# Performance work log

Measured on AMD Instinct MI355X. Metric: run time of the kernel, lower is better.

## Reference

```python
import jax, jax.numpy as jnp
import numpy as np

B, S, H, P, T = 8, 2048, 1024, 256, 4
EPS = 1e-12


def setup_inputs() -> dict:
    key = jax.random.key(0)
    ks = jax.random.split(key, 12)
    sd = 0.02
    return {
        "hidden_states": jax.random.normal(ks[0], (B, S, H), jnp.float32),
        "input_tensor": jax.random.normal(ks[1], (B, S, H), jnp.float32),
        "attention_mask": jnp.zeros((B, 1, 1, S), jnp.float32),
        "dense_W": jax.random.normal(ks[2], (H, H), jnp.float32) * sd,
        "dense_b": jnp.zeros((H,), jnp.float32),
        "pal_W1": jax.random.normal(ks[3], (T, H, P), jnp.float32) * sd,  # H2L per task
        "pal_b1": jnp.zeros((T, P), jnp.float32),
        "pal_W2": jax.random.normal(ks[4], (T, P, H), jnp.float32) * sd,  # L2H per task
        "pal_b2": jnp.zeros((T, H), jnp.float32),
        "enc_W": jax.random.normal(ks[5], (H,), jnp.float32) * sd,  # Linear(H,1)
        "enc_b": jnp.zeros((), jnp.float32),
        "sel_W": jax.random.normal(ks[6], (T, H), jnp.float32) * sd,  # Linear(H,T)
        "sel_b": jnp.zeros((T,), jnp.float32),
        "ln_g": jnp.ones((H,), jnp.float32),
        "ln_b": jnp.zeros((H,), jnp.float32),
    }


def reference(hidden_states, input_tensor, attention_mask, dense_W, dense_b,
              pal_W1, pal_b1, pal_W2, pal_b2, enc_W, enc_b, sel_W, sel_b,
              ln_g, ln_b):
    # dense projection (dropout p=0 -> identity)
    h = jnp.einsum('bsh,hk->bsk', hidden_states, dense_W) + dense_b  # [B,S,H]

    # per-task PAL adapters: H -> P -> H, stacked over T
    low = jnp.einsum('bsh,thp->btsp', h, pal_W1) + pal_b1[:, None, :]   # [B,T,S,P]
    task_specific = jnp.einsum('btsp,tph->btsh', low, pal_W2) + pal_b2[:, None, :]  # [B,T,S,H]

    # token-level gating: softmax over sequence of (encoder logits + additive mask)
    task_logits = jnp.einsum('bsh,h->bs', h, enc_W) + enc_b            # [B,S]
    task_weights = jax.nn.softmax(task_logits + attention_mask.reshape(B, S), axis=-1)
    task_vector = jnp.einsum('bs,bsh->bh', task_weights, h)            # [B,H]

    # task selector distribution and weighted combine over task branches
    task_distribution = jax.nn.softmax(task_vector @ sel_W.T + sel_b, axis=-1)  # [B,T]
    summed = jnp.einsum('btsh,bt->bsh', task_specific, task_distribution)       # [B,S,H]

    # residual + LayerNorm (eps=1e-12)
    x = h + input_tensor + summed
    mu = x.mean(-1, keepdims=True)
    var = ((x - mu) ** 2).mean(-1, keepdims=True)
    return ln_g * (x - mu) / jnp.sqrt(var + EPS) + ln_b
```

## Files before the change

kernel.cpp:

```cpp
#include <hip/hip_runtime.h>
#include <stdint.h>

#define DEVI __device__ __forceinline__

typedef __attribute__((ext_vector_type(8))) short s8v;
typedef __attribute__((ext_vector_type(4))) float f4v;
typedef unsigned short u16;

DEVI float bf2f(u16 u) { union { uint32_t i; float f; } c; c.i = ((uint32_t)u) << 16; return c.f; }
DEVI u16 f2bf(float f) {
  union { float f; uint32_t u; } c; c.f = f;
  uint32_t u = c.u;
  u += 0x7fffu + ((u >> 16) & 1u);
  return (u16)(u >> 16);
}

DEVI void gld16(const void* g, void* l) {
  auto gp = reinterpret_cast<const __attribute__((address_space(1))) void*>(reinterpret_cast<uintptr_t>(g));
  auto lp = reinterpret_cast<__attribute__((address_space(3))) void*>(reinterpret_cast<uintptr_t>(l));
  __builtin_amdgcn_global_load_lds(gp, lp, 16, 0, 0);
}

DEVI float wredsum(float v) {
  #pragma unroll
  for (int o = 32; o; o >>= 1) v += __shfl_xor(v, o);
  return v;
}

#define MFMA16(a, b, c) __builtin_amdgcn_mfma_f32_16x16x32_bf16((a), (b), (c), 0, 0, 0)

__global__ void cvt_f32_bf16(const float4* __restrict__ in, ushort4* __restrict__ out) {
  int i = blockIdx.x * 256 + threadIdx.x;
  float4 v = in[i];
  ushort4 o;
  o.x = f2bf(v.x); o.y = f2bf(v.y); o.z = f2bf(v.z); o.w = f2bf(v.w);
  out[i] = o;
}

__global__ void transpose_cvt(const float* __restrict__ in, u16* __restrict__ out, int R, int C) {
  __shared__ float t[32][33];
  in  += (size_t)blockIdx.z * R * C;
  out += (size_t)blockIdx.z * R * C;
  int r0 = blockIdx.y * 32, c0 = blockIdx.x * 32;
  int tx = threadIdx.x, ty = threadIdx.y;
  #pragma unroll
  for (int j = ty; j < 32; j += 8) t[j][tx] = in[(size_t)(r0 + j) * C + c0 + tx];
  __syncthreads();
  #pragma unroll
  for (int j = ty; j < 32; j += 8) out[(size_t)(c0 + j) * R + r0 + tx] = f2bf(t[tx][j]);
}


template<int EPI>
__global__ __launch_bounds__(256, 4) void gemm_bt(
    const u16* __restrict__ A, const u16* __restrict__ Bt, void* out,
    const float* __restrict__ e0, const float* __restrict__ e1, const u16* e2)
{
  const int tid  = threadIdx.x;
  const int lane = tid & 63;
  const int wv   = tid >> 6;
  const int wg = ((blockIdx.x & 7) << 7) | (blockIdx.x >> 3);
  const int tm = wg >> 3;
  const int tn = wg & 7;

  __shared__ char lds[32768];
  char* As = lds;
  char* Bs = lds + 16384;

  f4v acc[4][4];
  #pragma unroll
  for (int i = 0; i < 4; i++)
    #pragma unroll
    for (int j = 0; j < 4; j++) acc[i][j] = f4v{0.f, 0.f, 0.f, 0.f};

  const int wr = wv >> 1, wc = wv & 1;
  const int mB = wr * 64, nB = wc * 64;
  const int fr = lane & 15;
  const int fkbyte = (lane >> 4) << 4;

  const char* Ab = (const char*)(A + (size_t)tm * 128 * 1024);
  const char* Bb = (const char*)(Bt + (size_t)tn * 128 * 1024);

  for (int k0 = 0; k0 < 1024; k0 += 64) {
    #pragma unroll
    for (int c = 0; c < 4; ++c) {
      int p = wv * 1024 + lane * 16 + c * 4096;
      int row = p >> 7;
      int kb = (p & 127) ^ ((row & 7) << 4);
      gld16(Ab + (size_t)row * 2048 + k0 * 2 + kb, As + p);
      gld16(Bb + (size_t)row * 2048 + k0 * 2 + kb, Bs + p);
    }
    __syncthreads();
    #pragma unroll
    for (int kk = 0; kk < 2; ++kk) {
      s8v af[4], bf[4];
      #pragma unroll
      for (int i = 0; i < 4; ++i) {
        int ra = mB + i * 16 + fr;
        int rb = nB + i * 16 + fr;
        int kbyte = kk * 64 + fkbyte;
        af[i] = *(const s8v*)(As + ra * 128 + (kbyte ^ ((ra & 7) << 4)));
        bf[i] = *(const s8v*)(Bs + rb * 128 + (kbyte ^ ((rb & 7) << 4)));
      }
      #pragma unroll
      for (int mi = 0; mi < 4; ++mi)
        #pragma unroll
        for (int ni = 0; ni < 4; ++ni)
          acc[mi][ni] = MFMA16(af[mi], bf[ni], acc[mi][ni]);
    }
    __syncthreads();
  }

  const int mBase = tm * 128 + mB;
  const int nBase = tn * 128 + nB;
  const int rl = (lane >> 4) << 2;
  const int cl = lane & 15;
  float scale = 0.f;
  const float* b2row = nullptr;
  if constexpr (EPI == 2) scale = e1[(tm >> 4) * 4 + (tn >> 1)];
  if constexpr (EPI == 3) b2row = e0 + (tm >> 4) * 1024;

  #pragma unroll
  for (int mi = 0; mi < 4; ++mi) {
    #pragma unroll
    for (int ni = 0; ni < 4; ++ni) {
      int n = nBase + ni * 16 + cl;
      #pragma unroll
      for (int v = 0; v < 4; ++v) {
        int m = mBase + mi * 16 + rl + v;
        size_t idx = (size_t)m * 1024 + n;
        float val = acc[mi][ni][v];
        if constexpr (EPI == 1) {
          ((u16*)out)[idx] = f2bf(val + e0[n]);
        } else if constexpr (EPI == 2) {
          ((u16*)out)[idx] = f2bf(scale * (val + e0[n]));
        } else {
          ((u16*)out)[idx] = f2bf(val + b2row[n] + bf2f(e2[idx]) + e1[idx]);
        }
      }
    }
  }
}

template<int EPI>
__global__ __launch_bounds__(512, 6) void gemm_hi(
    const u16* __restrict__ A, const u16* __restrict__ Bt, void* out,
    const float* __restrict__ e0, const float* __restrict__ e1, const u16* e2)
{
  const int tid  = threadIdx.x;
  const int lane = tid & 63;
  const int wid  = tid >> 6;
  const int wm = wid >> 1, wn = wid & 1;
  const int wg = ((blockIdx.x & 7) << 7) | (blockIdx.x >> 3);
  const int tm = wg >> 3;
  const int tn = wg & 7;

  __shared__ char As[16384];
  __shared__ char Bs[16384];

  f4v acc[2][4];
  #pragma unroll
  for (int i = 0; i < 2; i++)
    #pragma unroll
    for (int j = 0; j < 4; j++) acc[i][j] = f4v{0.f, 0.f, 0.f, 0.f};

  const int mB = wm * 32, nB = wn * 64;
  const int fr = lane & 15;
  const int fkbyte = (lane >> 4) << 4;

  const char* Ab = (const char*)(A + (size_t)tm * 128 * 1024);
  const char* Bb = (const char*)(Bt + (size_t)tn * 128 * 1024);

  for (int k0 = 0; k0 < 1024; k0 += 64) {
    #pragma unroll
    for (int c = 0; c < 2; ++c) {
      int p = tid * 16 + c * 8192;
      int row = p >> 7;
      int kb = (p & 127) ^ ((row & 7) << 4);
      gld16(Ab + (size_t)row * 2048 + k0 * 2 + kb, As + p);
      gld16(Bb + (size_t)row * 2048 + k0 * 2 + kb, Bs + p);
    }
    __syncthreads();
    #pragma unroll
    for (int kk = 0; kk < 2; ++kk) {
      s8v af[2], bf[4];
      const int kbyte = kk * 64 + fkbyte;
      #pragma unroll
      for (int i = 0; i < 2; ++i) {
        int ra = mB + i * 16 + fr;
        af[i] = *(const s8v*)(As + ra * 128 + (kbyte ^ ((ra & 7) << 4)));
      }
      #pragma unroll
      for (int j = 0; j < 4; ++j) {
        int rb = nB + j * 16 + fr;
        bf[j] = *(const s8v*)(Bs + rb * 128 + (kbyte ^ ((rb & 7) << 4)));
      }
      #pragma unroll
      for (int i = 0; i < 2; ++i)
        #pragma unroll
        for (int j = 0; j < 4; ++j)
          acc[i][j] = MFMA16(af[i], bf[j], acc[i][j]);
    }
    __syncthreads();
  }

  const int mBase = tm * 128 + mB;
  const int nBase = tn * 128 + nB;
  const int rl = (lane >> 4) << 2;
  const int cl = lane & 15;
  float scale = 0.f;
  const float* b2row = nullptr;
  if constexpr (EPI == 2) scale = e1[(tm >> 4) * 4 + (tn >> 1)];
  if constexpr (EPI == 3) b2row = e0 + (tm >> 4) * 1024;

  #pragma unroll
  for (int i = 0; i < 2; ++i) {
    #pragma unroll
    for (int j = 0; j < 4; ++j) {
      int n = nBase + j * 16 + cl;
      #pragma unroll
      for (int v = 0; v < 4; ++v) {
        int m = mBase + i * 16 + rl + v;
        size_t idx = (size_t)m * 1024 + n;
        float val = acc[i][j][v];
        if constexpr (EPI == 1) {
          ((u16*)out)[idx] = f2bf(val + e0[n]);
        } else if constexpr (EPI == 2) {
          ((u16*)out)[idx] = f2bf(scale * (val + e0[n]));
        } else {
          ((u16*)out)[idx] = f2bf(val + b2row[n] + bf2f(e2[idx]) + e1[idx]);
        }
      }
    }
  }
}

__global__ void rowdot_kernel(const u16* __restrict__ h, const float* __restrict__ encW,
                              const float* __restrict__ encb, float* __restrict__ logits) {
  int row  = blockIdx.x * 4 + (threadIdx.x >> 6);
  int lane = threadIdx.x & 63;
  const u16* hp = h + (size_t)row * 1024 + lane * 16;
  s8v a0 = *(const s8v*)hp;
  s8v a1 = *(const s8v*)(hp + 8);
  const float* wp = encW + lane * 16;
  float s = 0.f;
  #pragma unroll
  for (int j = 0; j < 8; j++) s += bf2f((u16)a0[j]) * wp[j];
  #pragma unroll
  for (int j = 0; j < 8; j++) s += bf2f((u16)a1[j]) * wp[8 + j];
  s = wredsum(s);
  if (lane == 0) logits[row] = s + encb[0];
}

__global__ void softmax_seq(const float* __restrict__ logits, const float* __restrict__ mask,
                            float* __restrict__ w) {
  int b = blockIdx.x, tid = threadIdx.x;
  int lane = tid & 63, wv = tid >> 6;
  const float* lp = logits + (size_t)b * 2048;
  const float* mp = mask + (size_t)b * 2048;
  float v[8];
  #pragma unroll
  for (int i = 0; i < 8; i++) v[i] = lp[tid * 8 + i] + mp[tid * 8 + i];
  float mx = -1e30f;
  #pragma unroll
  for (int i = 0; i < 8; i++) mx = fmaxf(mx, v[i]);
  __shared__ float red[4];
  #pragma unroll
  for (int o = 32; o; o >>= 1) mx = fmaxf(mx, __shfl_xor(mx, o));
  if (lane == 0) red[wv] = mx;
  __syncthreads();
  mx = fmaxf(fmaxf(red[0], red[1]), fmaxf(red[2], red[3]));
  __syncthreads();
  float s = 0.f;
  #pragma unroll
  for (int i = 0; i < 8; i++) { v[i] = expf(v[i] - mx); s += v[i]; }
  s = wredsum(s);
  if (lane == 0) red[wv] = s;
  __syncthreads();
  s = red[0] + red[1] + red[2] + red[3];
  float inv = 1.f / s;
  #pragma unroll
  for (int i = 0; i < 8; i++) w[(size_t)b * 2048 + tid * 8 + i] = v[i] * inv;
}

__global__ void taskvec_part(const u16* __restrict__ h, const float* __restrict__ w,
                             float* __restrict__ tvp) {
  int b = blockIdx.y, sc = blockIdx.z;
  int col = blockIdx.x * 256 + threadIdx.x;
  const u16* hp = h + ((size_t)b * 2048 + sc * 256) * 1024 + col;
  const float* wp = w + (size_t)b * 2048 + sc * 256;
  float a0 = 0.f, a1 = 0.f, a2 = 0.f, a3 = 0.f;
  for (int s = 0; s < 256; s += 4) {
    a0 += wp[s]     * bf2f(hp[(size_t)s * 1024]);
    a1 += wp[s + 1] * bf2f(hp[(size_t)(s + 1) * 1024]);
    a2 += wp[s + 2] * bf2f(hp[(size_t)(s + 2) * 1024]);
    a3 += wp[s + 3] * bf2f(hp[(size_t)(s + 3) * 1024]);
  }
  tvp[((size_t)b * 8 + sc) * 1024 + col] = (a0 + a1) + (a2 + a3);
}

__global__ void taskvec_reduce(const float* __restrict__ tvp, float* __restrict__ tv) {
  int b = blockIdx.y;
  int col = blockIdx.x * 256 + threadIdx.x;
  float s = 0.f;
  #pragma unroll
  for (int c = 0; c < 8; c++) s += tvp[((size_t)b * 8 + c) * 1024 + col];
  tv[(size_t)b * 1024 + col] = s;
}

__global__ void taskdist_kernel(const float* __restrict__ tv, const float* __restrict__ selW,
                                const float* __restrict__ selb, const float* __restrict__ pb2,
                                float* __restrict__ dvec, float* __restrict__ bias2) {
  int b = blockIdx.x, tid = threadIdx.x;
  int lane = tid & 63, wv = tid >> 6;
  const float* tp = tv + (size_t)b * 1024;
  const float* sw = selW + (size_t)wv * 1024;
  float s = 0.f;
  #pragma unroll
  for (int j = 0; j < 16; j++) s += tp[lane * 16 + j] * sw[lane * 16 + j];
  s = wredsum(s);
  __shared__ float lg[4];
  if (lane == 0) lg[wv] = s + selb[wv];
  __syncthreads();
  float m = fmaxf(fmaxf(lg[0], lg[1]), fmaxf(lg[2], lg[3]));
  float e0 = expf(lg[0] - m), e1 = expf(lg[1] - m), e2 = expf(lg[2] - m), e3 = expf(lg[3] - m);
  float inv = 1.f / (e0 + e1 + e2 + e3);
  float d0 = e0 * inv, d1 = e1 * inv, d2 = e2 * inv, d3 = e3 * inv;
  if (tid < 4) dvec[b * 4 + tid] = (tid == 0) ? d0 : (tid == 1) ? d1 : (tid == 2) ? d2 : d3;
  #pragma unroll
  for (int c = 0; c < 4; c++) {
    int n = c * 256 + tid;
    bias2[(size_t)b * 1024 + n] =
        d0 * pb2[n] + d1 * pb2[1024 + n] + d2 * pb2[2048 + n] + d3 * pb2[3072 + n];
  }
}

__global__ void ln_bf16_kernel(const u16* __restrict__ x, const float* __restrict__ g,
                               const float* __restrict__ bt, float* __restrict__ out) {
  int row = blockIdx.x, tid = threadIdx.x;
  int lane = tid & 63, wv = tid >> 6;
  ushort4 u = ((const ushort4*)(x + (size_t)row * 1024))[tid];
  float v0 = bf2f(u.x), v1 = bf2f(u.y), v2 = bf2f(u.z), v3 = bf2f(u.w);
  float s = v0 + v1 + v2 + v3;
  float q = v0 * v0 + v1 * v1 + v2 * v2 + v3 * v3;
  #pragma unroll
  for (int o = 32; o; o >>= 1) { s += __shfl_xor(s, o); q += __shfl_xor(q, o); }
  __shared__ float rs[4], rq[4];
  if (lane == 0) { rs[wv] = s; rq[wv] = q; }
  __syncthreads();
  s = rs[0] + rs[1] + rs[2] + rs[3];
  q = rq[0] + rq[1] + rq[2] + rq[3];
  float mu = s * (1.f / 1024.f);
  float var = q * (1.f / 1024.f) - mu * mu;
  float inv = 1.f / sqrtf(var + 1e-12f);
  const float4 gv = ((const float4*)g)[tid];
  const float4 bv = ((const float4*)bt)[tid];
  float4 o;
  o.x = gv.x * (v0 - mu) * inv + bv.x;
  o.y = gv.y * (v1 - mu) * inv + bv.y;
  o.z = gv.z * (v2 - mu) * inv + bv.z;
  o.w = gv.w * (v3 - mu) * inv + bv.w;
  ((float4*)(out + (size_t)row * 1024))[tid] = o;
}

extern "C" void kernel_launch(void* const* d_in, const int* in_sizes, int n_in,
                              void* d_out, int out_size, void* d_ws, size_t ws_size,
                              hipStream_t stream) {
  const float* hidden = (const float*)d_in[0];
  const float* input  = (const float*)d_in[1];
  const float* mask   = (const float*)d_in[2];
  const float* denseW = (const float*)d_in[3];
  const float* denseB = (const float*)d_in[4];
  const float* palW1  = (const float*)d_in[5];
  const float* palB1  = (const float*)d_in[6];
  const float* palW2  = (const float*)d_in[7];
  const float* palB2  = (const float*)d_in[8];
  const float* encW   = (const float*)d_in[9];
  const float* encB   = (const float*)d_in[10];
  const float* selW   = (const float*)d_in[11];
  const float* selB   = (const float*)d_in[12];
  const float* lnG    = (const float*)d_in[13];
  const float* lnB    = (const float*)d_in[14];

  char* ws = (char*)d_ws;
  u16*  hbf    = (u16*)(ws);
  u16*  a0low  = (u16*)(ws + 33554432);
  u16*  wdt    = (u16*)(ws + 67108864);
  u16*  w1t    = (u16*)(ws + 69206016);
  u16*  w2t    = (u16*)(ws + 71303168);
  float* logits = (float*)(ws + 73400320);
  float* wts    = (float*)(ws + 73465856);
  float* tv     = (float*)(ws + 73531392);
  float* dvec   = (float*)(ws + 73564160);
  float* bias2  = (float*)(ws + 73568256);
  float* tvp    = (float*)(ws + 73601024);

  cvt_f32_bf16<<<16384, 256, 0, stream>>>((const float4*)hidden, (ushort4*)a0low);
  transpose_cvt<<<dim3(32, 32, 1), dim3(32, 8), 0, stream>>>(denseW, wdt, 1024, 1024);
  transpose_cvt<<<dim3(8, 32, 4),  dim3(32, 8), 0, stream>>>(palW1, w1t, 1024, 256);
  transpose_cvt<<<dim3(32, 32, 1), dim3(32, 8), 0, stream>>>(palW2, w2t, 1024, 1024);

  gemm_bt<1><<<1024, 256, 0, stream>>>(a0low, wdt, hbf, denseB, nullptr, nullptr);

  rowdot_kernel<<<4096, 256, 0, stream>>>(hbf, encW, encB, logits);
  softmax_seq<<<8, 256, 0, stream>>>(logits, mask, wts);
  taskvec_part<<<dim3(4, 8, 8), 256, 0, stream>>>(hbf, wts, tvp);
  taskvec_reduce<<<dim3(4, 8), 256, 0, stream>>>(tvp, tv);
  taskdist_kernel<<<8, 256, 0, stream>>>(tv, selW, selB, palB2, dvec, bias2);

  gemm_hi<2><<<1024, 512, 0, stream>>>(hbf, w1t, a0low, palB1, dvec, nullptr);
  gemm_bt<3><<<1024, 256, 0, stream>>>(a0low, w2t, hbf, bias2, input, hbf);

  ln_bf16_kernel<<<16384, 256, 0, stream>>>(hbf, lnG, lnB, (float*)d_out);
}
```

Before: 211.7 us.

## Fuse fp32 conversion and encoder logits into dense GEMM; merge taskvec reduce

The dense projection GEMM now reads fp32 hidden states directly, converting them to bf16 while staging A into LDS. This removes the separate conversion kernel and its intermediate buffer. The encoder row-dot is computed in the GEMM epilogue and accumulated into the logits with atomics, after a memset, which removes a full re-read of h. The encoder bias is dropped because softmax is shift-invariant. The taskvec partial reduction is folded into the task-distribution kernel. In exchange, A tiles now go through synchronous register loads instead of async LDS loads, which may add stalls, and atomics add contention.

```diff
diff --git a/kernel.cpp b/kernel.cpp
--- a/kernel.cpp
+++ b/kernel.cpp
@@ -5,6 +5,7 @@
 
 typedef __attribute__((ext_vector_type(8))) short s8v;
 typedef __attribute__((ext_vector_type(4))) float f4v;
+typedef __attribute__((ext_vector_type(4))) int i4v;
 typedef unsigned short u16;
 
 DEVI float bf2f(u16 u) { union { uint32_t i; float f; } c; c.i = ((uint32_t)u) << 16; return c.f; }
@@ -14,6 +15,9 @@
   u += 0x7fffu + ((u >> 16) & 1u);
   return (u16)(u >> 16);
 }
+DEVI uint32_t pk2bf(float a, float b) {
+  return (uint32_t)f2bf(a) | ((uint32_t)f2bf(b) << 16);
+}
 
 DEVI void gld16(const void* g, void* l) {
   auto gp = reinterpret_cast<const __attribute__((address_space(1))) void*>(reinterpret_cast<uintptr_t>(g));
@@ -28,14 +32,6 @@
 }
 
 #define MFMA16(a, b, c) __builtin_amdgcn_mfma_f32_16x16x32_bf16((a), (b), (c), 0, 0, 0)
-
-__global__ void cvt_f32_bf16(const float4* __restrict__ in, ushort4* __restrict__ out) {
-  int i = blockIdx.x * 256 + threadIdx.x;
-  float4 v = in[i];
-  ushort4 o;
-  o.x = f2bf(v.x); o.y = f2bf(v.y); o.z = f2bf(v.z); o.w = f2bf(v.w);
-  out[i] = o;
-}
 
 __global__ void transpose_cvt(const float* __restrict__ in, u16* __restrict__ out, int R, int C) {
   __shared__ float t[32][33];
@@ -50,6 +46,109 @@
   for (int j = ty; j < 32; j += 8) out[(size_t)(c0 + j) * R + r0 + tx] = f2bf(t[tx][j]);
 }
 
+
+__global__ __launch_bounds__(256, 4) void gemm_f32a(
+    const float* __restrict__ Af, const u16* __restrict__ Bt, u16* __restrict__ out,
+    const float* __restrict__ bias, const float* __restrict__ encW, float* __restrict__ logits)
+{
+  const int tid  = threadIdx.x;
+  const int lane = tid & 63;
+  const int wv   = tid >> 6;
+  const int wg = ((blockIdx.x & 7) << 7) | (blockIdx.x >> 3);
+  const int tm = wg >> 3;
+  const int tn = wg & 7;
+
+  __shared__ char lds[32768];
+  char* As = lds;
+  char* Bs = lds + 16384;
+
+  f4v acc[4][4];
+  #pragma unroll
+  for (int i = 0; i < 4; i++)
+    #pragma unroll
+    for (int j = 0; j < 4; j++) acc[i][j] = f4v{0.f, 0.f, 0.f, 0.f};
+
+  const int wr = wv >> 1, wc = wv & 1;
+  const int mB = wr * 64, nB = wc * 64;
+  const int fr = lane & 15;
+  const int fkbyte = (lane >> 4) << 4;
+
+  const float* Ab = Af + (size_t)tm * 128 * 1024;
+  const char*  Bb = (const char*)(Bt + (size_t)tn * 128 * 1024);
+
+  for (int k0 = 0; k0 < 1024; k0 += 64) {
+    #pragma unroll
+    for (int c = 0; c < 4; ++c) {
+      int p = wv * 1024 + lane * 16 + c * 4096;
+      int row = p >> 7;
+      int kb = (p & 127) ^ ((row & 7) << 4);
+      gld16(Bb + (size_t)row * 2048 + k0 * 2 + kb, Bs + p);
+    }
+    #pragma unroll
+    for (int c = 0; c < 4; ++c) {
+      int p = wv * 1024 + lane * 16 + c * 4096;
+      int row = p >> 7;
+      int colb = p & 127;
+      const float* src = Ab + (size_t)row * 1024 + k0 + (colb >> 1);
+      float4 x0 = *(const float4*)src;
+      float4 x1 = *(const float4*)(src + 4);
+      i4v w;
+      w[0] = (int)pk2bf(x0.x, x0.y);
+      w[1] = (int)pk2bf(x0.z, x0.w);
+      w[2] = (int)pk2bf(x1.x, x1.y);
+      w[3] = (int)pk2bf(x1.z, x1.w);
+      *(i4v*)(As + row * 128 + (colb ^ ((row & 7) << 4))) = w;
+    }
+    __syncthreads();
+    #pragma unroll
+    for (int kk = 0; kk < 2; ++kk) {
+      s8v af[4], bf[4];
+      #pragma unroll
+      for (int i = 0; i < 4; ++i) {
+        int ra = mB + i * 16 + fr;
+        int rb = nB + i * 16 + fr;
+        int kbyte = kk * 64 + fkbyte;
+        af[i] = *(const s8v*)(As + ra * 128 + (kbyte ^ ((ra & 7) << 4)));
+        bf[i] = *(const s8v*)(Bs + rb * 128 + (kbyte ^ ((rb & 7) << 4)));
+      }
+      #pragma unroll
+      for (int mi = 0; mi < 4; ++mi)
+        #pragma unroll
+        for (int ni = 0; ni < 4; ++ni)
+          acc[mi][ni] = MFMA16(af[mi], bf[ni], acc[mi][ni]);
+    }
+    __syncthreads();
+  }
+
+  const int mBase = tm * 128 + mB;
+  const int nBase = tn * 128 + nB;
+  const int rl = (lane >> 4) << 2;
+  const int cl = lane & 15;
+  float ew[4], bv[4];
+  #pragma unroll
+  for (int ni = 0; ni < 4; ++ni) {
+    ew[ni] = encW[nBase + ni * 16 + cl];
+    bv[ni] = bias[nBase + ni * 16 + cl];
+  }
+  #pragma unroll
+  for (int mi = 0; mi < 4; ++mi) {
+    #pragma unroll
+    for (int v = 0; v < 4; ++v) {
+      int m = mBase + mi * 16 + rl + v;
+      float dotp = 0.f;
+      #pragma unroll
+      for (int ni = 0; ni < 4; ++ni) {
+        int n = nBase + ni * 16 + cl;
+        float val = acc[mi][ni][v] + bv[ni];
+        out[(size_t)m * 1024 + n] = f2bf(val);
+        dotp += val * ew[ni];
+      }
+      #pragma unroll
+      for (int o = 1; o < 16; o <<= 1) dotp += __shfl_xor(dotp, o);
+      if (cl == 0) atomicAdd(&logits[m], dotp);
+    }
+  }
+}
 
 template<int EPI>
 __global__ __launch_bounds__(256, 4) void gemm_bt(
@@ -130,9 +229,7 @@
         int m = mBase + mi * 16 + rl + v;
         size_t idx = (size_t)m * 1024 + n;
         float val = acc[mi][ni][v];
-        if constexpr (EPI == 1) {
-          ((u16*)out)[idx] = f2bf(val + e0[n]);
-        } else if constexpr (EPI == 2) {
+        if constexpr (EPI == 2) {
           ((u16*)out)[idx] = f2bf(scale * (val + e0[n]));
         } else {
           ((u16*)out)[idx] = f2bf(val + b2row[n] + bf2f(e2[idx]) + e1[idx]);
@@ -223,9 +320,7 @@
         int m = mBase + i * 16 + rl + v;
         size_t idx = (size_t)m * 1024 + n;
         float val = acc[i][j][v];
-        if constexpr (EPI == 1) {
-          ((u16*)out)[idx] = f2bf(val + e0[n]);
-        } else if constexpr (EPI == 2) {
+        if constexpr (EPI == 2) {
           ((u16*)out)[idx] = f2bf(scale * (val + e0[n]));
         } else {
           ((u16*)out)[idx] = f2bf(val + b2row[n] + bf2f(e2[idx]) + e1[idx]);
@@ -233,23 +328,6 @@
       }
     }
   }
-}
-
-__global__ void rowdot_kernel(const u16* __restrict__ h, const float* __restrict__ encW,
-                              const float* __restrict__ encb, float* __restrict__ logits) {
-  int row  = blockIdx.x * 4 + (threadIdx.x >> 6);
-  int lane = threadIdx.x & 63;
-  const u16* hp = h + (size_t)row * 1024 + lane * 16;
-  s8v a0 = *(const s8v*)hp;
-  s8v a1 = *(const s8v*)(hp + 8);
-  const float* wp = encW + lane * 16;
-  float s = 0.f;
-  #pragma unroll
-  for (int j = 0; j < 8; j++) s += bf2f((u16)a0[j]) * wp[j];
-  #pragma unroll
-  for (int j = 0; j < 8; j++) s += bf2f((u16)a1[j]) * wp[8 + j];
-  s = wredsum(s);
-  if (lane == 0) logits[row] = s + encb[0];
 }
 
 __global__ void softmax_seq(const float* __restrict__ logits, const float* __restrict__ mask,
@@ -299,25 +377,25 @@
   tvp[((size_t)b * 8 + sc) * 1024 + col] = (a0 + a1) + (a2 + a3);
 }
 
-__global__ void taskvec_reduce(const float* __restrict__ tvp, float* __restrict__ tv) {
-  int b = blockIdx.y;
-  int col = blockIdx.x * 256 + threadIdx.x;
-  float s = 0.f;
-  #pragma unroll
-  for (int c = 0; c < 8; c++) s += tvp[((size_t)b * 8 + c) * 1024 + col];
-  tv[(size_t)b * 1024 + col] = s;
-}
-
-__global__ void taskdist_kernel(const float* __restrict__ tv, const float* __restrict__ selW,
-                                const float* __restrict__ selb, const float* __restrict__ pb2,
-                                float* __restrict__ dvec, float* __restrict__ bias2) {
+__global__ void taskvec_dist(const float* __restrict__ tvp, const float* __restrict__ selW,
+                             const float* __restrict__ selb, const float* __restrict__ pb2,
+                             float* __restrict__ dvec, float* __restrict__ bias2) {
   int b = blockIdx.x, tid = threadIdx.x;
   int lane = tid & 63, wv = tid >> 6;
-  const float* tp = tv + (size_t)b * 1024;
+  __shared__ float tvs[1024];
+  #pragma unroll
+  for (int c4 = 0; c4 < 4; ++c4) {
+    int col = c4 * 256 + tid;
+    float s = 0.f;
+    #pragma unroll
+    for (int c = 0; c < 8; ++c) s += tvp[((size_t)b * 8 + c) * 1024 + col];
+    tvs[col] = s;
+  }
+  __syncthreads();
   const float* sw = selW + (size_t)wv * 1024;
   float s = 0.f;
   #pragma unroll
-  for (int j = 0; j < 16; j++) s += tp[lane * 16 + j] * sw[lane * 16 + j];
+  for (int j = 0; j < 16; j++) s += tvs[lane * 16 + j] * sw[lane * 16 + j];
   s = wredsum(s);
   __shared__ float lg[4];
   if (lane == 0) lg[wv] = s + selb[wv];
@@ -376,7 +454,6 @@
   const float* palW2  = (const float*)d_in[7];
   const float* palB2  = (const float*)d_in[8];
   const float* encW   = (const float*)d_in[9];
-  const float* encB   = (const float*)d_in[10];
   const float* selW   = (const float*)d_in[11];
   const float* selB   = (const float*)d_in[12];
   const float* lnG    = (const float*)d_in[13];
@@ -384,32 +461,29 @@
 
   char* ws = (char*)d_ws;
   u16*  hbf    = (u16*)(ws);
-  u16*  a0low  = (u16*)(ws + 33554432);
+  u16*  lowbuf = (u16*)(ws + 33554432);
   u16*  wdt    = (u16*)(ws + 67108864);
   u16*  w1t    = (u16*)(ws + 69206016);
   u16*  w2t    = (u16*)(ws + 71303168);
   float* logits = (float*)(ws + 73400320);
   float* wts    = (float*)(ws + 73465856);
-  float* tv     = (float*)(ws + 73531392);
   float* dvec   = (float*)(ws + 73564160);
   float* bias2  = (float*)(ws + 73568256);
   float* tvp    = (float*)(ws + 73601024);
 
-  cvt_f32_bf16<<<16384, 256, 0, stream>>>((const float4*)hidden, (ushort4*)a0low);
   transpose_cvt<<<dim3(32, 32, 1), dim3(32, 8), 0, stream>>>(denseW, wdt, 1024, 1024);
   transpose_cvt<<<dim3(8, 32, 4),  dim3(32, 8), 0, stream>>>(palW1, w1t, 1024, 256);
   transpose_cvt<<<dim3(32, 32, 1), dim3(32, 8), 0, stream>>>(palW2, w2t, 1024, 1024);
-
-  gemm_bt<1><<<1024, 256, 0, stream>>>(a0low, wdt, hbf, denseB, nullptr, nullptr);
-
-  rowdot_kernel<<<4096, 256, 0, stream>>>(hbf, encW, encB, logits);
+  hipMemsetAsync(logits, 0, 16384 * sizeof(float), stream);
+
+  gemm_f32a<<<1024, 256, 0, stream>>>(hidden, wdt, hbf, denseB, encW, logits);
+
   softmax_seq<<<8, 256, 0, stream>>>(logits, mask, wts);
   taskvec_part<<<dim3(4, 8, 8), 256, 0, stream>>>(hbf, wts, tvp);
-  taskvec_reduce<<<dim3(4, 8), 256, 0, stream>>>(tvp, tv);
-  taskdist_kernel<<<8, 256, 0, stream>>>(tv, selW, selB, palB2, dvec, bias2);
-
-  gemm_hi<2><<<1024, 512, 0, stream>>>(hbf, w1t, a0low, palB1, dvec, nullptr);
-  gemm_bt<3><<<1024, 256, 0, stream>>>(a0low, w2t, hbf, bias2, input, hbf);
+  taskvec_dist<<<8, 256, 0, stream>>>(tvp, selW, selB, palB2, dvec, bias2);
+
+  gemm_hi<2><<<1024, 512, 0, stream>>>(hbf, w1t, lowbuf, palB1, dvec, nullptr);
+  gemm_bt<3><<<1024, 256, 0, stream>>>(lowbuf, w2t, hbf, bias2, input, hbf);
 
   ln_bf16_kernel<<<16384, 256, 0, stream>>>(hbf, lnG, lnB, (float*)d_out);
 }
```

Measured after the change: 239.7 us. 13.2% more time.

## Fuse encoder logits into dense GEMM epilogue and use 512-thread GEMM variant

Applied to the files above, without the earlier changes.

The dense projection GEMM now runs as a 512-thread kernel whose epilogue also computes per-row partial dot products with enc_W. These partials are written per column tile into the output buffer used as scratch, and the sequence softmax sums them. This removes the separate rowdot pass that re-read h. The taskvec reduce and task-distribution kernels are merged into one, and the final adapter GEMM switches from gemm_bt to the gemm_hi tiling. The enc_b bias is dropped, which is valid because a constant shift cancels in the sequence softmax; the trade-off is a heavier epilogue and an extra block-level sync in the GEMM.

```diff
diff --git a/kernel.cpp b/kernel.cpp
--- a/kernel.cpp
+++ b/kernel.cpp
@@ -51,30 +51,29 @@
 }
 
 
-template<int EPI>
-__global__ __launch_bounds__(256, 4) void gemm_bt(
-    const u16* __restrict__ A, const u16* __restrict__ Bt, void* out,
-    const float* __restrict__ e0, const float* __restrict__ e1, const u16* e2)
+__global__ __launch_bounds__(512, 6) void gemm_hi1(
+    const u16* __restrict__ A, const u16* __restrict__ Bt, u16* __restrict__ out,
+    const float* __restrict__ bias, const float* __restrict__ encW, float* __restrict__ part)
 {
   const int tid  = threadIdx.x;
   const int lane = tid & 63;
-  const int wv   = tid >> 6;
+  const int wid  = tid >> 6;
+  const int wm = wid >> 1, wn = wid & 1;
   const int wg = ((blockIdx.x & 7) << 7) | (blockIdx.x >> 3);
   const int tm = wg >> 3;
   const int tn = wg & 7;
 
-  __shared__ char lds[32768];
-  char* As = lds;
-  char* Bs = lds + 16384;
-
-  f4v acc[4][4];
-  #pragma unroll
-  for (int i = 0; i < 4; i++)
+  __shared__ char As[16384];
+  __shared__ char Bs[16384];
+  __shared__ float redbuf[128];
+
+  f4v acc[2][4];
+  #pragma unroll
+  for (int i = 0; i < 2; i++)
     #pragma unroll
     for (int j = 0; j < 4; j++) acc[i][j] = f4v{0.f, 0.f, 0.f, 0.f};
 
-  const int wr = wv >> 1, wc = wv & 1;
-  const int mB = wr * 64, nB = wc * 64;
+  const int mB = wm * 32, nB = wn * 64;
   const int fr = lane & 15;
   const int fkbyte = (lane >> 4) << 4;
 
@@ -83,8 +82,8 @@
 
   for (int k0 = 0; k0 < 1024; k0 += 64) {
     #pragma unroll
-    for (int c = 0; c < 4; ++c) {
-      int p = wv * 1024 + lane * 16 + c * 4096;
+    for (int c = 0; c < 2; ++c) {
+      int p = tid * 16 + c * 8192;
       int row = p >> 7;
       int kb = (p & 127) ^ ((row & 7) << 4);
       gld16(Ab + (size_t)row * 2048 + k0 * 2 + kb, As + p);
@@ -93,20 +92,23 @@
     __syncthreads();
     #pragma unroll
     for (int kk = 0; kk < 2; ++kk) {
-      s8v af[4], bf[4];
-      #pragma unroll
-      for (int i = 0; i < 4; ++i) {
+      s8v af[2], bf[4];
+      const int kbyte = kk * 64 + fkbyte;
+      #pragma unroll
+      for (int i = 0; i < 2; ++i) {
         int ra = mB + i * 16 + fr;
-        int rb = nB + i * 16 + fr;
-        int kbyte = kk * 64 + fkbyte;
         af[i] = *(const s8v*)(As + ra * 128 + (kbyte ^ ((ra & 7) << 4)));
-        bf[i] = *(const s8v*)(Bs + rb * 128 + (kbyte ^ ((rb & 7) << 4)));
-      }
-      #pragma unroll
-      for (int mi = 0; mi < 4; ++mi)
+      }
+      #pragma unroll
+      for (int j = 0; j < 4; ++j) {
+        int rb = nB + j * 16 + fr;
+        bf[j] = *(const s8v*)(Bs + rb * 128 + (kbyte ^ ((rb & 7) << 4)));
+      }
+      #pragma unroll
+      for (int i = 0; i < 2; ++i)
         #pragma unroll
-        for (int ni = 0; ni < 4; ++ni)
-          acc[mi][ni] = MFMA16(af[mi], bf[ni], acc[mi][ni]);
+        for (int j = 0; j < 4; ++j)
+          acc[i][j] = MFMA16(af[i], bf[j], acc[i][j]);
     }
     __syncthreads();
   }
@@ -115,30 +117,35 @@
   const int nBase = tn * 128 + nB;
   const int rl = (lane >> 4) << 2;
   const int cl = lane & 15;
-  float scale = 0.f;
-  const float* b2row = nullptr;
-  if constexpr (EPI == 2) scale = e1[(tm >> 4) * 4 + (tn >> 1)];
-  if constexpr (EPI == 3) b2row = e0 + (tm >> 4) * 1024;
-
-  #pragma unroll
-  for (int mi = 0; mi < 4; ++mi) {
-    #pragma unroll
-    for (int ni = 0; ni < 4; ++ni) {
-      int n = nBase + ni * 16 + cl;
+  float md[2][4];
+  #pragma unroll
+  for (int i = 0; i < 2; ++i) {
+    #pragma unroll
+    for (int v = 0; v < 4; ++v) {
+      int m = mBase + i * 16 + rl + v;
+      float dotp = 0.f;
+      #pragma unroll
+      for (int ni = 0; ni < 4; ++ni) {
+        int n = nBase + ni * 16 + cl;
+        float val = acc[i][ni][v] + bias[n];
+        out[(size_t)m * 1024 + n] = f2bf(val);
+        dotp += val * encW[n];
+      }
+      #pragma unroll
+      for (int o = 1; o < 16; o <<= 1) dotp += __shfl_xor(dotp, o);
+      md[i][v] = dotp;
+      if (wn == 0 && cl == 0) redbuf[mB + i * 16 + rl + v] = dotp;
+    }
+  }
+  __syncthreads();
+  if (wn == 1 && cl == 0) {
+    #pragma unroll
+    for (int i = 0; i < 2; ++i)
       #pragma unroll
       for (int v = 0; v < 4; ++v) {
-        int m = mBase + mi * 16 + rl + v;
-        size_t idx = (size_t)m * 1024 + n;
-        float val = acc[mi][ni][v];
-        if constexpr (EPI == 1) {
-          ((u16*)out)[idx] = f2bf(val + e0[n]);
-        } else if constexpr (EPI == 2) {
-          ((u16*)out)[idx] = f2bf(scale * (val + e0[n]));
-        } else {
-          ((u16*)out)[idx] = f2bf(val + b2row[n] + bf2f(e2[idx]) + e1[idx]);
-        }
-      }
-    }
+        int ml = mB + i * 16 + rl + v;
+        part[(size_t)tn * 16384 + tm * 128 + ml] = redbuf[ml] + md[i][v];
+      }
   }
 }
 
@@ -223,9 +230,7 @@
         int m = mBase + i * 16 + rl + v;
         size_t idx = (size_t)m * 1024 + n;
         float val = acc[i][j][v];
-        if constexpr (EPI == 1) {
-          ((u16*)out)[idx] = f2bf(val + e0[n]);
-        } else if constexpr (EPI == 2) {
+        if constexpr (EPI == 2) {
           ((u16*)out)[idx] = f2bf(scale * (val + e0[n]));
         } else {
           ((u16*)out)[idx] = f2bf(val + b2row[n] + bf2f(e2[idx]) + e1[idx]);
@@ -235,32 +240,20 @@
   }
 }
 
-__global__ void rowdot_kernel(const u16* __restrict__ h, const float* __restrict__ encW,
-                              const float* __restrict__ encb, float* __restrict__ logits) {
-  int row  = blockIdx.x * 4 + (threadIdx.x >> 6);
-  int lane = threadIdx.x & 63;
-  const u16* hp = h + (size_t)row * 1024 + lane * 16;
-  s8v a0 = *(const s8v*)hp;
-  s8v a1 = *(const s8v*)(hp + 8);
-  const float* wp = encW + lane * 16;
-  float s = 0.f;
-  #pragma unroll
-  for (int j = 0; j < 8; j++) s += bf2f((u16)a0[j]) * wp[j];
-  #pragma unroll
-  for (int j = 0; j < 8; j++) s += bf2f((u16)a1[j]) * wp[8 + j];
-  s = wredsum(s);
-  if (lane == 0) logits[row] = s + encb[0];
-}
-
-__global__ void softmax_seq(const float* __restrict__ logits, const float* __restrict__ mask,
+__global__ void softmax_seq(const float* __restrict__ part, const float* __restrict__ mask,
                             float* __restrict__ w) {
   int b = blockIdx.x, tid = threadIdx.x;
   int lane = tid & 63, wv = tid >> 6;
-  const float* lp = logits + (size_t)b * 2048;
   const float* mp = mask + (size_t)b * 2048;
   float v[8];
   #pragma unroll
-  for (int i = 0; i < 8; i++) v[i] = lp[tid * 8 + i] + mp[tid * 8 + i];
+  for (int i = 0; i < 8; i++) {
+    int row = b * 2048 + tid * 8 + i;
+    float s = 0.f;
+    #pragma unroll
+    for (int t = 0; t < 8; t++) s += part[(size_t)t * 16384 + row];
+    v[i] = s + mp[tid * 8 + i];
+  }
   float mx = -1e30f;
   #pragma unroll
   for (int i = 0; i < 8; i++) mx = fmaxf(mx, v[i]);
@@ -299,25 +292,25 @@
   tvp[((size_t)b * 8 + sc) * 1024 + col] = (a0 + a1) + (a2 + a3);
 }
 
-__global__ void taskvec_reduce(const float* __restrict__ tvp, float* __restrict__ tv) {
-  int b = blockIdx.y;
-  int col = blockIdx.x * 256 + threadIdx.x;
-  float s = 0.f;
-  #pragma unroll
-  for (int c = 0; c < 8; c++) s += tvp[((size_t)b * 8 + c) * 1024 + col];
-  tv[(size_t)b * 1024 + col] = s;
-}
-
-__global__ void taskdist_kernel(const float* __restrict__ tv, const float* __restrict__ selW,
-                                const float* __restrict__ selb, const float* __restrict__ pb2,
-                                float* __restrict__ dvec, float* __restrict__ bias2) {
+__global__ void taskvec_dist(const float* __restrict__ tvp, const float* __restrict__ selW,
+                             const float* __restrict__ selb, const float* __restrict__ pb2,
+                             float* __restrict__ dvec, float* __restrict__ bias2) {
   int b = blockIdx.x, tid = threadIdx.x;
   int lane = tid & 63, wv = tid >> 6;
-  const float* tp = tv + (size_t)b * 1024;
+  __shared__ float tvs[1024];
+  #pragma unroll
+  for (int c4 = 0; c4 < 4; ++c4) {
+    int col = c4 * 256 + tid;
+    float s = 0.f;
+    #pragma unroll
+    for (int c = 0; c < 8; ++c) s += tvp[((size_t)b * 8 + c) * 1024 + col];
+    tvs[col] = s;
+  }
+  __syncthreads();
   const float* sw = selW + (size_t)wv * 1024;
   float s = 0.f;
   #pragma unroll
-  for (int j = 0; j < 16; j++) s += tp[lane * 16 + j] * sw[lane * 16 + j];
+  for (int j = 0; j < 16; j++) s += tvs[lane * 16 + j] * sw[lane * 16 + j];
   s = wredsum(s);
   __shared__ float lg[4];
   if (lane == 0) lg[wv] = s + selb[wv];
@@ -376,7 +369,6 @@
   const float* palW2  = (const float*)d_in[7];
   const float* palB2  = (const float*)d_in[8];
   const float* encW   = (const float*)d_in[9];
-  const float* encB   = (const float*)d_in[10];
   const float* selW   = (const float*)d_in[11];
   const float* selB   = (const float*)d_in[12];
   const float* lnG    = (const float*)d_in[13];
@@ -384,32 +376,30 @@
 
   char* ws = (char*)d_ws;
   u16*  hbf    = (u16*)(ws);
-  u16*  a0low  = (u16*)(ws + 33554432);
+  u16*  lowbuf = (u16*)(ws + 33554432);
   u16*  wdt    = (u16*)(ws + 67108864);
   u16*  w1t    = (u16*)(ws + 69206016);
   u16*  w2t    = (u16*)(ws + 71303168);
-  float* logits = (float*)(ws + 73400320);
   float* wts    = (float*)(ws + 73465856);
-  float* tv     = (float*)(ws + 73531392);
   float* dvec   = (float*)(ws + 73564160);
   float* bias2  = (float*)(ws + 73568256);
   float* tvp    = (float*)(ws + 73601024);
 
-  cvt_f32_bf16<<<16384, 256, 0, stream>>>((const float4*)hidden, (ushort4*)a0low);
+  float* lgpart = (float*)d_out;
+
+  cvt_f32_bf16<<<16384, 256, 0, stream>>>((const float4*)hidden, (ushort4*)lowbuf);
   transpose_cvt<<<dim3(32, 32, 1), dim3(32, 8), 0, stream>>>(denseW, wdt, 1024, 1024);
   transpose_cvt<<<dim3(8, 32, 4),  dim3(32, 8), 0, stream>>>(palW1, w1t, 1024, 256);
   transpose_cvt<<<dim3(32, 32, 1), dim3(32, 8), 0, stream>>>(palW2, w2t, 1024, 1024);
 
-  gemm_bt<1><<<1024, 256, 0, stream>>>(a0low, wdt, hbf, denseB, nullptr, nullptr);
-
-  rowdot_kernel<<<4096, 256, 0, stream>>>(hbf, encW, encB, logits);
-  softmax_seq<<<8, 256, 0, stream>>>(logits, mask, wts);
+  gemm_hi1<<<1024, 512, 0, stream>>>(lowbuf, wdt, hbf, denseB, encW, lgpart);
+
+  softmax_seq<<<8, 256, 0, stream>>>(lgpart, mask, wts);
   taskvec_part<<<dim3(4, 8, 8), 256, 0, stream>>>(hbf, wts, tvp);
-  taskvec_reduce<<<dim3(4, 8), 256, 0, stream>>>(tvp, tv);
-  taskdist_kernel<<<8, 256, 0, stream>>>(tv, selW, selB, palB2, dvec, bias2);
-
-  gemm_hi<2><<<1024, 512, 0, stream>>>(hbf, w1t, a0low, palB1, dvec, nullptr);
-  gemm_bt<3><<<1024, 256, 0, stream>>>(a0low, w2t, hbf, bias2, input, hbf);
+  taskvec_dist<<<8, 256, 0, stream>>>(tvp, selW, selB, palB2, dvec, bias2);
+
+  gemm_hi<2><<<1024, 512, 0, stream>>>(hbf, w1t, lowbuf, palB1, dvec, nullptr);
+  gemm_hi<3><<<1024, 512, 0, stream>>>(lowbuf, w2t, hbf, bias2, input, hbf);
 
   ln_bf16_kernel<<<16384, 256, 0, stream>>>(hbf, lnG, lnB, (float*)d_out);
 }
```

After: 242.3 us. 1.14x slower.
